# Kernel tuning notes

Hardware: AMD Instinct MI355X
Metric: run time of the kernel (lower is better)

The kernel has to match this reference:

```python
import jax, jax.numpy as jnp
import numpy as np

N_NODES = 50000
N_EDGES = 800000
D = 128


def gcn_conv(x, W, b, src, dst, num_nodes):
    """PyG GCNConv: x @ W, add self-loops, symmetric normalization, scatter-add, + bias."""
    x = x @ W  # [N, out]
    loop = jnp.arange(num_nodes, dtype=src.dtype)
    s = jnp.concatenate([src, loop])  # [E+N]
    d = jnp.concatenate([dst, loop])
    w = jnp.ones(s.shape[0], x.dtype)  # edge_weight=None -> ones (self-loop fill=1)
    deg = jax.ops.segment_sum(w, d, num_segments=num_nodes)  # [N]
    dinv = jnp.where(deg > 0, jax.lax.rsqrt(deg), 0.0)
    norm = dinv[s] * dinv[d]  # [E+N]
    out = jax.ops.segment_sum(x[s] * norm[:, None], d, num_segments=num_nodes)
    return out + b


def setup_inputs() -> dict:
    key = jax.random.key(0)
    ks = jax.random.split(key, 8)
    sc = 1.0 / np.sqrt(D)
    x = jax.random.normal(ks[0], (N_NODES, D), dtype=jnp.float32)
    edge_index = jax.random.randint(ks[1], (2, N_EDGES), 0, N_NODES)
    W1 = jax.random.normal(ks[2], (D, D), dtype=jnp.float32) * sc
    W2 = jax.random.normal(ks[3], (D, D), dtype=jnp.float32) * sc
    W3 = jax.random.normal(ks[4], (D, D), dtype=jnp.float32) * sc
    b1 = jnp.zeros((D,), jnp.float32)
    b2 = jnp.zeros((D,), jnp.float32)
    b3 = jnp.zeros((D,), jnp.float32)
    return {"x": x, "edge_index": edge_index, "W1": W1, "b1": b1,
            "W2": W2, "b2": b2, "W3": W3, "b3": b3}


def reference(x, edge_index, W1, b1, W2, b2, W3, b3):
    src, dst = edge_index[0], edge_index[1]
    n = x.shape[0]
    x = jax.nn.relu(gcn_conv(x, W1, b1, src, dst, n))
    x = jax.nn.relu(gcn_conv(x, W2, b2, src, dst, n))
    return gcn_conv(x, W3, b3, src, dst, n)
```

## Files before the change

### kernel.cpp

```cpp
#include <hip/hip_runtime.h>
#include <hip/hip_fp16.h>
#include <math.h>

#define D 128
#define PADH 136

typedef __attribute__((ext_vector_type(8))) _Float16 half8;
typedef __attribute__((ext_vector_type(4))) float f32x4;


__global__ void prep_kernel(const float* __restrict__ W1, const float* __restrict__ W2,
                            const float* __restrict__ W3, __half* __restrict__ WhT,
                            int* __restrict__ cnt, int N) {
    int i = blockIdx.x * blockDim.x + threadIdx.x;
    if (i < 3 * D * D) {
        int l = i >> 14, j = i & 16383, n = j >> 7, k = j & 127;
        const float* W = (l == 0) ? W1 : (l == 1) ? W2 : W3;
        WhT[(size_t)i] = __float2half(W[(size_t)k * D + n]);
    }
    if (i < N) cnt[i] = 0;
}


__global__ void count_rank_kernel(const int* __restrict__ dst, int* __restrict__ cnt,
                                  int* __restrict__ rank, int E) {
    int e0 = (blockIdx.x * blockDim.x + threadIdx.x) * 8;
    if (e0 + 7 < E) {
        int4 da = *(const int4*)(dst + e0);
        int4 db = *(const int4*)(dst + e0 + 4);
        int4 ra, rb;
        ra.x = atomicAdd(&cnt[da.x], 1);
        ra.y = atomicAdd(&cnt[da.y], 1);
        ra.z = atomicAdd(&cnt[da.z], 1);
        ra.w = atomicAdd(&cnt[da.w], 1);
        rb.x = atomicAdd(&cnt[db.x], 1);
        rb.y = atomicAdd(&cnt[db.y], 1);
        rb.z = atomicAdd(&cnt[db.z], 1);
        rb.w = atomicAdd(&cnt[db.w], 1);
        *(int4*)(rank + e0)     = ra;
        *(int4*)(rank + e0 + 4) = rb;
    } else {
        for (int e = e0; e < E; ++e) rank[e] = atomicAdd(&cnt[dst[e]], 1);
    }
}

__global__ __launch_bounds__(1024) void scan_kernel(const int* __restrict__ cnt,
                                                    int* __restrict__ rowptr,
                                                    float* __restrict__ dinv,
                                                    int N) {
    __shared__ int wsum[16];
    int tid  = threadIdx.x;
    int lane = tid & 63;
    int wid  = tid >> 6;
    int C = ((N + 4095) / 4096) * 4;
    int start = tid * C;
    int end   = start + C; if (end > N) end = N;

    int local = 0;
    int i = start;
    for (; i + 3 < end; i += 4) {
        int4 v = *(const int4*)(cnt + i);
        local += v.x + v.y + v.z + v.w;
    }
    for (; i < end; ++i) local += cnt[i];

    int sc = local;
    #pragma unroll
    for (int off = 1; off < 64; off <<= 1) {
        int t = __shfl_up(sc, off, 64);
        if (lane >= off) sc += t;
    }
    if (lane == 63) wsum[wid] = sc;
    __syncthreads();
    if (tid < 16) {
        int w = wsum[tid];
        #pragma unroll
        for (int off = 1; off < 16; off <<= 1) {
            int t = __shfl_up(w, off, 16);
            if (tid >= off) w += t;
        }
        wsum[tid] = w;
    }
    __syncthreads();
    int run = ((wid > 0) ? wsum[wid - 1] : 0) + (sc - local);

    i = start;
    for (; i + 3 < end; i += 4) {
        int4 v = *(const int4*)(cnt + i);
        int4 rp;
        rp.x = run; rp.y = rp.x + v.x; rp.z = rp.y + v.y; rp.w = rp.z + v.z;
        run = rp.w + v.w;
        *(int4*)(rowptr + i) = rp;
        float4 dv;
        dv.x = rsqrtf((float)v.x + 1.0f);
        dv.y = rsqrtf((float)v.y + 1.0f);
        dv.z = rsqrtf((float)v.z + 1.0f);
        dv.w = rsqrtf((float)v.w + 1.0f);
        *(float4*)(dinv + i) = dv;
    }
    for (; i < end; ++i) {
        int v = cnt[i];
        rowptr[i] = run; run += v;
        dinv[i] = rsqrtf((float)v + 1.0f);
    }
    if (tid == 0) rowptr[N] = wsum[15];
}


__device__ __forceinline__ void gather4(const __half* __restrict__ g,
                                        const int* __restrict__ rowptr,
                                        const int* __restrict__ col,
                                        int row, int lane, float* __restrict__ acc) {
    int grp = lane >> 4;
    int l16 = lane & 15;
    int gb  = grp << 4;
    int s = rowptr[row], e = rowptr[row + 1];

    half8 hs = ((const half8*)(g + (size_t)row * D))[l16];
    float a0 = (float)hs[0], a1 = (float)hs[1], a2 = (float)hs[2], a3 = (float)hs[3];
    float a4 = (float)hs[4], a5 = (float)hs[5], a6 = (float)hs[6], a7 = (float)hs[7];
    float b0 = 0.f, b1 = 0.f, b2 = 0.f, b3 = 0.f, b4 = 0.f, b5 = 0.f, b6 = 0.f, b7 = 0.f;

    for (int base = s; base < e; base += 16) {
        int idx = base + l16;
        int myc = (idx < e) ? col[idx] : 0;
        int nb  = min(16, e - base);
        int j = 0;
        for (; j + 8 <= nb; j += 8) {
            int c0 = __shfl(myc, gb + j + 0), c1 = __shfl(myc, gb + j + 1);
            int c2 = __shfl(myc, gb + j + 2), c3 = __shfl(myc, gb + j + 3);
            int c4 = __shfl(myc, gb + j + 4), c5 = __shfl(myc, gb + j + 5);
            int c6 = __shfl(myc, gb + j + 6), c7 = __shfl(myc, gb + j + 7);
            half8 v0 = ((const half8*)(g + (size_t)c0 * D))[l16];
            half8 v1 = ((const half8*)(g + (size_t)c1 * D))[l16];
            half8 v2 = ((const half8*)(g + (size_t)c2 * D))[l16];
            half8 v3 = ((const half8*)(g + (size_t)c3 * D))[l16];
            half8 v4 = ((const half8*)(g + (size_t)c4 * D))[l16];
            half8 v5 = ((const half8*)(g + (size_t)c5 * D))[l16];
            half8 v6 = ((const half8*)(g + (size_t)c6 * D))[l16];
            half8 v7 = ((const half8*)(g + (size_t)c7 * D))[l16];
            a0 += (float)v0[0]; a1 += (float)v0[1]; a2 += (float)v0[2]; a3 += (float)v0[3];
            a4 += (float)v0[4]; a5 += (float)v0[5]; a6 += (float)v0[6]; a7 += (float)v0[7];
            b0 += (float)v1[0]; b1 += (float)v1[1]; b2 += (float)v1[2]; b3 += (float)v1[3];
            b4 += (float)v1[4]; b5 += (float)v1[5]; b6 += (float)v1[6]; b7 += (float)v1[7];
            a0 += (float)v2[0]; a1 += (float)v2[1]; a2 += (float)v2[2]; a3 += (float)v2[3];
            a4 += (float)v2[4]; a5 += (float)v2[5]; a6 += (float)v2[6]; a7 += (float)v2[7];
            b0 += (float)v3[0]; b1 += (float)v3[1]; b2 += (float)v3[2]; b3 += (float)v3[3];
            b4 += (float)v3[4]; b5 += (float)v3[5]; b6 += (float)v3[6]; b7 += (float)v3[7];
            a0 += (float)v4[0]; a1 += (float)v4[1]; a2 += (float)v4[2]; a3 += (float)v4[3];
            a4 += (float)v4[4]; a5 += (float)v4[5]; a6 += (float)v4[6]; a7 += (float)v4[7];
            b0 += (float)v5[0]; b1 += (float)v5[1]; b2 += (float)v5[2]; b3 += (float)v5[3];
            b4 += (float)v5[4]; b5 += (float)v5[5]; b6 += (float)v5[6]; b7 += (float)v5[7];
            a0 += (float)v6[0]; a1 += (float)v6[1]; a2 += (float)v6[2]; a3 += (float)v6[3];
            a4 += (float)v6[4]; a5 += (float)v6[5]; a6 += (float)v6[6]; a7 += (float)v6[7];
            b0 += (float)v7[0]; b1 += (float)v7[1]; b2 += (float)v7[2]; b3 += (float)v7[3];
            b4 += (float)v7[4]; b5 += (float)v7[5]; b6 += (float)v7[6]; b7 += (float)v7[7];
        }
        for (; j + 4 <= nb; j += 4) {
            int c0 = __shfl(myc, gb + j + 0), c1 = __shfl(myc, gb + j + 1);
            int c2 = __shfl(myc, gb + j + 2), c3 = __shfl(myc, gb + j + 3);
            half8 v0 = ((const half8*)(g + (size_t)c0 * D))[l16];
            half8 v1 = ((const half8*)(g + (size_t)c1 * D))[l16];
            half8 v2 = ((const half8*)(g + (size_t)c2 * D))[l16];
            half8 v3 = ((const half8*)(g + (size_t)c3 * D))[l16];
            a0 += (float)v0[0]; a1 += (float)v0[1]; a2 += (float)v0[2]; a3 += (float)v0[3];
            a4 += (float)v0[4]; a5 += (float)v0[5]; a6 += (float)v0[6]; a7 += (float)v0[7];
            b0 += (float)v1[0]; b1 += (float)v1[1]; b2 += (float)v1[2]; b3 += (float)v1[3];
            b4 += (float)v1[4]; b5 += (float)v1[5]; b6 += (float)v1[6]; b7 += (float)v1[7];
            a0 += (float)v2[0]; a1 += (float)v2[1]; a2 += (float)v2[2]; a3 += (float)v2[3];
            a4 += (float)v2[4]; a5 += (float)v2[5]; a6 += (float)v2[6]; a7 += (float)v2[7];
            b0 += (float)v3[0]; b1 += (float)v3[1]; b2 += (float)v3[2]; b3 += (float)v3[3];
            b4 += (float)v3[4]; b5 += (float)v3[5]; b6 += (float)v3[6]; b7 += (float)v3[7];
        }
        for (; j < nb; ++j) {
            int c = __shfl(myc, gb + j);
            half8 v = ((const half8*)(g + (size_t)c * D))[l16];
            a0 += (float)v[0]; a1 += (float)v[1]; a2 += (float)v[2]; a3 += (float)v[3];
            a4 += (float)v[4]; a5 += (float)v[5]; a6 += (float)v[6]; a7 += (float)v[7];
        }
    }
    acc[0] = a0 + b0; acc[1] = a1 + b1; acc[2] = a2 + b2; acc[3] = a3 + b3;
    acc[4] = a4 + b4; acc[5] = a5 + b5; acc[6] = a6 + b6; acc[7] = a7 + b7;
}


__global__ __launch_bounds__(256) void fill_gemm1_kernel(
    const int* __restrict__ src, const int* __restrict__ dst,
    const int* __restrict__ rank, const int* __restrict__ rowptr,
    int* __restrict__ col, int E, int fill_blocks, int N,
    const float* __restrict__ X, const __half* __restrict__ WhT,
    const float* __restrict__ dinv, __half* __restrict__ Y, int M) {
    int tid = threadIdx.x;
    if ((int)blockIdx.x < fill_blocks) {
        int shard = blockIdx.x & 7;
        int sub   = blockIdx.x >> 3;
        int nsub  = fill_blocks >> 3;
        int chunk = (N + 7) >> 3;
        int lo = shard * chunk;
        unsigned span = (unsigned)(min(lo + chunk, N) - lo);
        const int NO = (E + 7) / 8;
        for (int c = sub * 256 + tid; c < NO; c += nsub * 256) {
            int e0 = c * 8;
            if (e0 + 7 < E) {
                int4 da = *(const int4*)(dst + e0);
                int4 db = *(const int4*)(dst + e0 + 4);
                bool i0 = (unsigned)(da.x - lo) < span, i1 = (unsigned)(da.y - lo) < span;
                bool i2 = (unsigned)(da.z - lo) < span, i3 = (unsigned)(da.w - lo) < span;
                bool i4 = (unsigned)(db.x - lo) < span, i5 = (unsigned)(db.y - lo) < span;
                bool i6 = (unsigned)(db.z - lo) < span, i7 = (unsigned)(db.w - lo) < span;
                if (i0 | i1 | i2 | i3 | i4 | i5 | i6 | i7) {
                    int4 ra = *(const int4*)(rank + e0);
                    int4 rb = *(const int4*)(rank + e0 + 4);
                    int4 sa = *(const int4*)(src + e0);
                    int4 sb = *(const int4*)(src + e0 + 4);
                    if (i0) col[rowptr[da.x] + ra.x] = sa.x;
                    if (i1) col[rowptr[da.y] + ra.y] = sa.y;
                    if (i2) col[rowptr[da.z] + ra.z] = sa.z;
                    if (i3) col[rowptr[da.w] + ra.w] = sa.w;
                    if (i4) col[rowptr[db.x] + rb.x] = sb.x;
                    if (i5) col[rowptr[db.y] + rb.y] = sb.y;
                    if (i6) col[rowptr[db.z] + rb.z] = sb.z;
                    if (i7) col[rowptr[db.w] + rb.w] = sb.w;
                }
            } else {
                for (int e = e0; e < E; ++e) {
                    int d = dst[e];
                    if ((unsigned)(d - lo) < span) col[rowptr[d] + rank[e]] = src[e];
                }
            }
        }
        return;
    }
    int bid  = blockIdx.x - fill_blocks;
    int wave = tid >> 6;
    int lane = tid & 63;
    int quad = lane >> 4;
    int l16  = lane & 15;
    int m0   = bid * 64 + wave * 16;
    if (m0 >= M) return;

    f32x4 acc[8];
    #pragma unroll
    for (int t = 0; t < 8; ++t) acc[t] = (f32x4)0.0f;
    const float* xrow = X + (size_t)(m0 + l16) * D;
    #pragma unroll
    for (int ks = 0; ks < 4; ++ks) {
        int k0 = ks * 32 + quad * 8;
        float4 x0 = *(const float4*)(xrow + k0);
        float4 x1 = *(const float4*)(xrow + k0 + 4);
        half8 a;
        a[0] = (_Float16)x0.x; a[1] = (_Float16)x0.y;
        a[2] = (_Float16)x0.z; a[3] = (_Float16)x0.w;
        a[4] = (_Float16)x1.x; a[5] = (_Float16)x1.y;
        a[6] = (_Float16)x1.z; a[7] = (_Float16)x1.w;
        #pragma unroll
        for (int t = 0; t < 8; ++t) {
            half8 b = *(const half8*)(WhT + (size_t)(t * 16 + l16) * D + k0);
            acc[t] = __builtin_amdgcn_mfma_f32_16x16x32_f16(a, b, acc[t], 0, 0, 0);
        }
    }
    float4 dv = *(const float4*)(dinv + m0 + quad * 4);
    float dvs[4] = {dv.x, dv.y, dv.z, dv.w};
    #pragma unroll
    for (int t = 0; t < 8; ++t) {
        #pragma unroll
        for (int r = 0; r < 4; ++r) {
            int grow = m0 + quad * 4 + r;
            Y[(size_t)grow * D + t * 16 + l16] = __float2half(acc[t][r] * dvs[r]);
        }
    }
}


__global__ __launch_bounds__(256) void agg_gemm_kernel(
    const __half* __restrict__ ysIn, const int* __restrict__ rowptr,
    const int* __restrict__ col, const float* __restrict__ dinv,
    const float* __restrict__ bias, const __half* __restrict__ WhT,
    __half* __restrict__ ysOut, int M) {
    __shared__ __half lds_h[16 * PADH];
    int tid  = threadIdx.x;
    int wave = tid >> 6;
    int lane = tid & 63;
    int grp  = lane >> 4;
    int l16  = lane & 15;
    int rbase = blockIdx.x * 16;
    int lrow  = wave * 4 + grp;
    int row   = min(rbase + lrow, M - 1);

    float acc8[8];
    gather4(ysIn, rowptr, col, row, lane, acc8);

    float dv = dinv[row];
    float4 bb0 = ((const float4*)bias)[l16 * 2];
    float4 bb1 = ((const float4*)bias)[l16 * 2 + 1];
    half8 hv;
    hv[0] = (_Float16)fmaxf(bb0.x + dv * acc8[0], 0.f);
    hv[1] = (_Float16)fmaxf(bb0.y + dv * acc8[1], 0.f);
    hv[2] = (_Float16)fmaxf(bb0.z + dv * acc8[2], 0.f);
    hv[3] = (_Float16)fmaxf(bb0.w + dv * acc8[3], 0.f);
    hv[4] = (_Float16)fmaxf(bb1.x + dv * acc8[4], 0.f);
    hv[5] = (_Float16)fmaxf(bb1.y + dv * acc8[5], 0.f);
    hv[6] = (_Float16)fmaxf(bb1.z + dv * acc8[6], 0.f);
    hv[7] = (_Float16)fmaxf(bb1.w + dv * acc8[7], 0.f);
    ((half8*)(lds_h + (size_t)lrow * PADH))[l16] = hv;
    __syncthreads();

    int quad = lane >> 4;
    int t0   = wave * 2;
    f32x4 acc0 = (f32x4)0.0f, acc1 = (f32x4)0.0f;
    const __half* arow = lds_h + (size_t)l16 * PADH;
    #pragma unroll
    for (int ks = 0; ks < 4; ++ks) {
        int k0 = ks * 32 + quad * 8;
        half8 a  = *(const half8*)(arow + k0);
        half8 b0 = *(const half8*)(WhT + (size_t)((t0 + 0) * 16 + l16) * D + k0);
        half8 b1 = *(const half8*)(WhT + (size_t)((t0 + 1) * 16 + l16) * D + k0);
        acc0 = __builtin_amdgcn_mfma_f32_16x16x32_f16(a, b0, acc0, 0, 0, 0);
        acc1 = __builtin_amdgcn_mfma_f32_16x16x32_f16(a, b1, acc1, 0, 0, 0);
    }
    #pragma unroll
    for (int r = 0; r < 4; ++r) {
        int grow = rbase + quad * 4 + r;
        if (grow < M) {
            float dvr = dinv[grow];
            ysOut[(size_t)grow * D + (t0 + 0) * 16 + l16] = __float2half(acc0[r] * dvr);
            ysOut[(size_t)grow * D + (t0 + 1) * 16 + l16] = __float2half(acc1[r] * dvr);
        }
    }
}


__global__ __launch_bounds__(256) void agg_final_kernel(
    const __half* __restrict__ ys, const int* __restrict__ rowptr,
    const int* __restrict__ col, const float* __restrict__ dinv,
    const float* __restrict__ b, float* __restrict__ out, int N) {
    int gwave = (blockIdx.x * blockDim.x + threadIdx.x) >> 6;
    int lane  = threadIdx.x & 63;
    int grp   = lane >> 4;
    int l16   = lane & 15;
    int rbase = gwave * 4;
    if (rbase >= N) return;
    int row = min(rbase + grp, N - 1);

    float acc8[8];
    gather4(ys, rowptr, col, row, lane, acc8);

    if (rbase + grp < N) {
        float dv = dinv[row];
        float4 bb0 = ((const float4*)b)[l16 * 2];
        float4 bb1 = ((const float4*)b)[l16 * 2 + 1];
        float4 r0, r1;
        r0.x = bb0.x + dv * acc8[0];
        r0.y = bb0.y + dv * acc8[1];
        r0.z = bb0.z + dv * acc8[2];
        r0.w = bb0.w + dv * acc8[3];
        r1.x = bb1.x + dv * acc8[4];
        r1.y = bb1.y + dv * acc8[5];
        r1.z = bb1.z + dv * acc8[6];
        r1.w = bb1.w + dv * acc8[7];
        float* op = out + (size_t)row * D + l16 * 8;
        ((float4*)op)[0] = r0;
        ((float4*)op)[1] = r1;
    }
}


extern "C" void kernel_launch(void* const* d_in, const int* in_sizes, int n_in,
                              void* d_out, int out_size, void* d_ws, size_t ws_size,
                              hipStream_t stream) {
    const float* x   = (const float*)d_in[0];
    const int*   ei  = (const int*)d_in[1];
    const float* W1  = (const float*)d_in[2];
    const float* b1  = (const float*)d_in[3];
    const float* W2  = (const float*)d_in[4];
    const float* b2  = (const float*)d_in[5];
    const float* W3  = (const float*)d_in[6];
    const float* b3  = (const float*)d_in[7];
    float* out = (float*)d_out;

    const int N = in_sizes[0] / D;
    const int E = in_sizes[1] / 2;
    const int* src = ei;
    const int* dst = ei + E;

    char* ws = (char*)d_ws;
    size_t off = 0;
    auto alloc = [&](size_t bytes) {
        void* p = ws + off;
        off = (off + bytes + 255) & ~(size_t)255;
        return p;
    };
    __half* ys    = (__half*)alloc((size_t)N * D * sizeof(__half));
    __half* hs    = (__half*)alloc((size_t)N * D * sizeof(__half));
    int*   cnt    = (int*)alloc((size_t)N * sizeof(int));
    int*   rowptr = (int*)alloc((size_t)(N + 1) * sizeof(int));
    float* dinv   = (float*)alloc((size_t)N * sizeof(float));
    int*   rank   = (int*)alloc((size_t)E * sizeof(int));
    int*   col    = (int*)alloc((size_t)E * sizeof(int));
    __half* WhT   = (__half*)alloc((size_t)3 * D * D * sizeof(__half));
    (void)ws_size; (void)n_in; (void)out_size;

    int prep_threads = (3 * D * D > N) ? 3 * D * D : N;
    prep_kernel<<<(prep_threads + 255) / 256, 256, 0, stream>>>(W1, W2, W3, WhT, cnt, N);

    const int NO = (E + 7) / 8;
    const int egrid = (NO + 255) / 256;
    count_rank_kernel<<<egrid, 256, 0, stream>>>(dst, cnt, rank, E);
    scan_kernel<<<1, 1024, 0, stream>>>(cnt, rowptr, dinv, N);

    const int FB = ((egrid + 7) / 8) * 8;
    const int gemm1_grid = (N + 63) / 64;
    fill_gemm1_kernel<<<FB + gemm1_grid, 256, 0, stream>>>(
        src, dst, rank, rowptr, col, E, FB, N, x, WhT, dinv, ys, N);

    const int agg_gemm_grid = (N + 15) / 16;
    agg_gemm_kernel<<<agg_gemm_grid, 256, 0, stream>>>(ys, rowptr, col, dinv, b1, WhT + 16384, hs, N);
    agg_gemm_kernel<<<agg_gemm_grid, 256, 0, stream>>>(hs, rowptr, col, dinv, b2, WhT + 32768, ys, N);

    const int aggf_grid = (((N + 3) / 4) * 64 + 255) / 256;
    agg_final_kernel<<<aggf_grid, 256, 0, stream>>>(ys, rowptr, col, dinv, b3, out, N);
}
```

Measured before the change: 298.0 us.

## Overlap first-layer GEMM with degree counting and unroll gather by sixteen

Moves the layer-1 X@W1 GEMM into the same launch as the edge degree-count atomics. It writes an fp32 intermediate, and a later fill kernel scales that intermediate by dinv and converts it to fp16 alongside the CSR fill. This lets the GEMM overlap the atomic counting phase instead of waiting for the scan. The gather loop also handles full 16-neighbor batches with 16 outstanding loads. The cost is an extra fp32 N×D buffer round trip, and the new path is used only when the workspace is large enough.

Result: slower. 310.3 us (+4.1%).

```diff
diff --git a/kernel.cpp b/kernel.cpp
--- a/kernel.cpp
+++ b/kernel.cpp
@@ -19,6 +19,405 @@
         WhT[(size_t)i] = __float2half(W[(size_t)k * D + n]);
     }
     if (i < N) cnt[i] = 0;
+}
+
+
+__global__ __launch_bounds__(256) void count_gemm1_kernel(
+    const int* __restrict__ dst, int* __restrict__ cnt, int* __restrict__ rank,
+    int E, int count_blocks,
+    const float* __restrict__ X, const __half* __restrict__ WhT,
+    float* __restrict__ Yf, int M) {
+    int tid = threadIdx.x;
+    if ((int)blockIdx.x < count_blocks) {
+        const int NO = (E + 7) / 8;
+        const int stride = count_blocks * 256;
+        for (int c = blockIdx.x * 256 + tid; c < NO; c += stride) {
+            int e0 = c * 8;
+            if (e0 + 7 < E) {
+                int4 da = *(const int4*)(dst + e0);
+                int4 db = *(const int4*)(dst + e0 + 4);
+                int4 ra, rb;
+                ra.x = atomicAdd(&cnt[da.x], 1);
+                ra.y = atomicAdd(&cnt[da.y], 1);
+                ra.z = atomicAdd(&cnt[da.z], 1);
+                ra.w = atomicAdd(&cnt[da.w], 1);
+                rb.x = atomicAdd(&cnt[db.x], 1);
+                rb.y = atomicAdd(&cnt[db.y], 1);
+                rb.z = atomicAdd(&cnt[db.z], 1);
+                rb.w = atomicAdd(&cnt[db.w], 1);
+                *(int4*)(rank + e0)     = ra;
+                *(int4*)(rank + e0 + 4) = rb;
+            } else {
+                for (int e = e0; e < E; ++e) rank[e] = atomicAdd(&cnt[dst[e]], 1);
+            }
+        }
+        return;
+    }
+    int bid  = blockIdx.x - count_blocks;
+    int wave = tid >> 6;
+    int lane = tid & 63;
+    int quad = lane >> 4;
+    int l16  = lane & 15;
+    int m0   = bid * 64 + wave * 16;
+    if (m0 >= M) return;
+
+    f32x4 acc[8];
+    #pragma unroll
+    for (int t = 0; t < 8; ++t) acc[t] = (f32x4)0.0f;
+    const float* xrow = X + (size_t)(m0 + l16) * D;
+    #pragma unroll
+    for (int ks = 0; ks < 4; ++ks) {
+        int k0 = ks * 32 + quad * 8;
+        float4 x0 = *(const float4*)(xrow + k0);
+        float4 x1 = *(const float4*)(xrow + k0 + 4);
+        half8 a;
+        a[0] = (_Float16)x0.x; a[1] = (_Float16)x0.y;
+        a[2] = (_Float16)x0.z; a[3] = (_Float16)x0.w;
+        a[4] = (_Float16)x1.x; a[5] = (_Float16)x1.y;
+        a[6] = (_Float16)x1.z; a[7] = (_Float16)x1.w;
+        #pragma unroll
+        for (int t = 0; t < 8; ++t) {
+            half8 b = *(const half8*)(WhT + (size_t)(t * 16 + l16) * D + k0);
+            acc[t] = __builtin_amdgcn_mfma_f32_16x16x32_f16(a, b, acc[t], 0, 0, 0);
+        }
+    }
+    #pragma unroll
+    for (int t = 0; t < 8; ++t) {
+        #pragma unroll
+        for (int r = 0; r < 4; ++r) {
+            int grow = m0 + quad * 4 + r;
+            Yf[(size_t)grow * D + t * 16 + l16] = acc[t][r];
+        }
+    }
+}
+
+
+__global__ __launch_bounds__(1024) void scan_kernel(const int* __restrict__ cnt,
+                                                    int* __restrict__ rowptr,
+                                                    float* __restrict__ dinv,
+                                                    int N) {
+    __shared__ int wsum[16];
+    int tid  = threadIdx.x;
+    int lane = tid & 63;
+    int wid  = tid >> 6;
+    int C = ((N + 4095) / 4096) * 4;
+    int start = tid * C;
+    int end   = start + C; if (end > N) end = N;
+
+    int local = 0;
+    int i = start;
+    for (; i + 3 < end; i += 4) {
+        int4 v = *(const int4*)(cnt + i);
+        local += v.x + v.y + v.z + v.w;
+    }
+    for (; i < end; ++i) local += cnt[i];
+
+    int sc = local;
+    #pragma unroll
+    for (int off = 1; off < 64; off <<= 1) {
+        int t = __shfl_up(sc, off, 64);
+        if (lane >= off) sc += t;
+    }
+    if (lane == 63) wsum[wid] = sc;
+    __syncthreads();
+    if (tid < 16) {
+        int w = wsum[tid];
+        #pragma unroll
+        for (int off = 1; off < 16; off <<= 1) {
+            int t = __shfl_up(w, off, 16);
+            if (tid >= off) w += t;
+        }
+        wsum[tid] = w;
+    }
+    __syncthreads();
+    int run = ((wid > 0) ? wsum[wid - 1] : 0) + (sc - local);
+
+    i = start;
+    for (; i + 3 < end; i += 4) {
+        int4 v = *(const int4*)(cnt + i);
+        int4 rp;
+        rp.x = run; rp.y = rp.x + v.x; rp.z = rp.y + v.y; rp.w = rp.z + v.z;
+        run = rp.w + v.w;
+        *(int4*)(rowptr + i) = rp;
+        float4 dv;
+        dv.x = rsqrtf((float)v.x + 1.0f);
+        dv.y = rsqrtf((float)v.y + 1.0f);
+        dv.z = rsqrtf((float)v.z + 1.0f);
+        dv.w = rsqrtf((float)v.w + 1.0f);
+        *(float4*)(dinv + i) = dv;
+    }
+    for (; i < end; ++i) {
+        int v = cnt[i];
+        rowptr[i] = run; run += v;
+        dinv[i] = rsqrtf((float)v + 1.0f);
+    }
+    if (tid == 0) rowptr[N] = wsum[15];
+}
+
+
+__global__ __launch_bounds__(256) void fill_scale_kernel(
+    const int* __restrict__ src, const int* __restrict__ dst,
+    const int* __restrict__ rank, const int* __restrict__ rowptr,
+    int* __restrict__ col, int E, int fill_blocks, int N,
+    const float* __restrict__ Yf, const float* __restrict__ dinv,
+    __half* __restrict__ Y, int scale_blocks) {
+    int tid = threadIdx.x;
+    if ((int)blockIdx.x < fill_blocks) {
+        int shard = blockIdx.x & 7;
+        int sub   = blockIdx.x >> 3;
+        int nsub  = fill_blocks >> 3;
+        int chunk = (N + 7) >> 3;
+        int lo = shard * chunk;
+        unsigned span = (unsigned)(min(lo + chunk, N) - lo);
+        const int NO = (E + 7) / 8;
+        for (int c = sub * 256 + tid; c < NO; c += nsub * 256) {
+            int e0 = c * 8;
+            if (e0 + 7 < E) {
+                int4 da = *(const int4*)(dst + e0);
+                int4 db = *(const int4*)(dst + e0 + 4);
+                bool i0 = (unsigned)(da.x - lo) < span, i1 = (unsigned)(da.y - lo) < span;
+                bool i2 = (unsigned)(da.z - lo) < span, i3 = (unsigned)(da.w - lo) < span;
+                bool i4 = (unsigned)(db.x - lo) < span, i5 = (unsigned)(db.y - lo) < span;
+                bool i6 = (unsigned)(db.z - lo) < span, i7 = (unsigned)(db.w - lo) < span;
+                if (i0 | i1 | i2 | i3 | i4 | i5 | i6 | i7) {
+                    int4 ra = *(const int4*)(rank + e0);
+                    int4 rb = *(const int4*)(rank + e0 + 4);
+                    int4 sa = *(const int4*)(src + e0);
+                    int4 sb = *(const int4*)(src + e0 + 4);
+                    if (i0) col[rowptr[da.x] + ra.x] = sa.x;
+                    if (i1) col[rowptr[da.y] + ra.y] = sa.y;
+                    if (i2) col[rowptr[da.z] + ra.z] = sa.z;
+                    if (i3) col[rowptr[da.w] + ra.w] = sa.w;
+                    if (i4) col[rowptr[db.x] + rb.x] = sb.x;
+                    if (i5) col[rowptr[db.y] + rb.y] = sb.y;
+                    if (i6) col[rowptr[db.z] + rb.z] = sb.z;
+                    if (i7) col[rowptr[db.w] + rb.w] = sb.w;
+                }
+            } else {
+                for (int e = e0; e < E; ++e) {
+                    int d = dst[e];
+                    if ((unsigned)(d - lo) < span) col[rowptr[d] + rank[e]] = src[e];
+                }
+            }
+        }
+        return;
+    }
+    int sb = blockIdx.x - fill_blocks;
+    const int nchunk = N * 16;
+    const int stride = scale_blocks * 256;
+    for (int i = sb * 256 + tid; i < nchunk; i += stride) {
+        int row = i >> 4;
+        int c8  = (i & 15) * 8;
+        const float* p = Yf + (size_t)row * D + c8;
+        float4 x0 = *(const float4*)p;
+        float4 x1 = *(const float4*)(p + 4);
+        float dv = dinv[row];
+        half8 h;
+        h[0] = (_Float16)(x0.x * dv); h[1] = (_Float16)(x0.y * dv);
+        h[2] = (_Float16)(x0.z * dv); h[3] = (_Float16)(x0.w * dv);
+        h[4] = (_Float16)(x1.x * dv); h[5] = (_Float16)(x1.y * dv);
+        h[6] = (_Float16)(x1.z * dv); h[7] = (_Float16)(x1.w * dv);
+        *(half8*)(Y + (size_t)row * D + c8) = h;
+    }
+}
+
+
+__device__ __forceinline__ void gather4(const __half* __restrict__ g,
+                                        const int* __restrict__ rowptr,
+                                        const int* __restrict__ col,
+                                        int row, int lane, float* __restrict__ acc) {
+    int grp = lane >> 4;
+    int l16 = lane & 15;
+    int gb  = grp << 4;
+    int s = rowptr[row], e = rowptr[row + 1];
+
+    half8 hs = ((const half8*)(g + (size_t)row * D))[l16];
+    float a0 = (float)hs[0], a1 = (float)hs[1], a2 = (float)hs[2], a3 = (float)hs[3];
+    float a4 = (float)hs[4], a5 = (float)hs[5], a6 = (float)hs[6], a7 = (float)hs[7];
+    float b0 = 0.f, b1 = 0.f, b2 = 0.f, b3 = 0.f, b4 = 0.f, b5 = 0.f, b6 = 0.f, b7 = 0.f;
+
+    for (int base = s; base < e; base += 16) {
+        int idx = base + l16;
+        int myc = (idx < e) ? col[idx] : 0;
+        int nb  = min(16, e - base);
+        if (nb == 16) {
+            int c0 = __shfl(myc, gb + 0),  c1 = __shfl(myc, gb + 1);
+            int c2 = __shfl(myc, gb + 2),  c3 = __shfl(myc, gb + 3);
+            int c4 = __shfl(myc, gb + 4),  c5 = __shfl(myc, gb + 5);
+            int c6 = __shfl(myc, gb + 6),  c7 = __shfl(myc, gb + 7);
+            int c8 = __shfl(myc, gb + 8),  c9 = __shfl(myc, gb + 9);
+            int cA = __shfl(myc, gb + 10), cB = __shfl(myc, gb + 11);
+            int cC = __shfl(myc, gb + 12), cD = __shfl(myc, gb + 13);
+            int cE = __shfl(myc, gb + 14), cF = __shfl(myc, gb + 15);
+            half8 v0 = ((const half8*)(g + (size_t)c0 * D))[l16];
+            half8 v1 = ((const half8*)(g + (size_t)c1 * D))[l16];
+            half8 v2 = ((const half8*)(g + (size_t)c2 * D))[l16];
+            half8 v3 = ((const half8*)(g + (size_t)c3 * D))[l16];
+            half8 v4 = ((const half8*)(g + (size_t)c4 * D))[l16];
+            half8 v5 = ((const half8*)(g + (size_t)c5 * D))[l16];
+            half8 v6 = ((const half8*)(g + (size_t)c6 * D))[l16];
+            half8 v7 = ((const half8*)(g + (size_t)c7 * D))[l16];
+            half8 v8 = ((const half8*)(g + (size_t)c8 * D))[l16];
+            half8 v9 = ((const half8*)(g + (size_t)c9 * D))[l16];
+            half8 vA = ((const half8*)(g + (size_t)cA * D))[l16];
+            half8 vB = ((const half8*)(g + (size_t)cB * D))[l16];
+            half8 vC = ((const half8*)(g + (size_t)cC * D))[l16];
+            half8 vD = ((const half8*)(g + (size_t)cD * D))[l16];
+            half8 vE = ((const half8*)(g + (size_t)cE * D))[l16];
+            half8 vF = ((const half8*)(g + (size_t)cF * D))[l16];
+            a0 += (float)v0[0]; a1 += (float)v0[1]; a2 += (float)v0[2]; a3 += (float)v0[3];
+            a4 += (float)v0[4]; a5 += (float)v0[5]; a6 += (float)v0[6]; a7 += (float)v0[7];
+            b0 += (float)v1[0]; b1 += (float)v1[1]; b2 += (float)v1[2]; b3 += (float)v1[3];
+            b4 += (float)v1[4]; b5 += (float)v1[5]; b6 += (float)v1[6]; b7 += (float)v1[7];
+            a0 += (float)v2[0]; a1 += (float)v2[1]; a2 += (float)v2[2]; a3 += (float)v2[3];
+            a4 += (float)v2[4]; a5 += (float)v2[5]; a6 += (float)v2[6]; a7 += (float)v2[7];
+            b0 += (float)v3[0]; b1 += (float)v3[1]; b2 += (float)v3[2]; b3 += (float)v3[3];
+            b4 += (float)v3[4]; b5 += (float)v3[5]; b6 += (float)v3[6]; b7 += (float)v3[7];
+            a0 += (float)v4[0]; a1 += (float)v4[1]; a2 += (float)v4[2]; a3 += (float)v4[3];
+            a4 += (float)v4[4]; a5 += (float)v4[5]; a6 += (float)v4[6]; a7 += (float)v4[7];
+            b0 += (float)v5[0]; b1 += (float)v5[1]; b2 += (float)v5[2]; b3 += (float)v5[3];
+            b4 += (float)v5[4]; b5 += (float)v5[5]; b6 += (float)v5[6]; b7 += (float)v5[7];
+            a0 += (float)v6[0]; a1 += (float)v6[1]; a2 += (float)v6[2]; a3 += (float)v6[3];
+            a4 += (float)v6[4]; a5 += (float)v6[5]; a6 += (float)v6[6]; a7 += (float)v6[7];
+            b0 += (float)v7[0]; b1 += (float)v7[1]; b2 += (float)v7[2]; b3 += (float)v7[3];
+            b4 += (float)v7[4]; b5 += (float)v7[5]; b6 += (float)v7[6]; b7 += (float)v7[7];
+            a0 += (float)v8[0]; a1 += (float)v8[1]; a2 += (float)v8[2]; a3 += (float)v8[3];
+            a4 += (float)v8[4]; a5 += (float)v8[5]; a6 += (float)v8[6]; a7 += (float)v8[7];
+            b0 += (float)v9[0]; b1 += (float)v9[1]; b2 += (float)v9[2]; b3 += (float)v9[3];
+            b4 += (float)v9[4]; b5 += (float)v9[5]; b6 += (float)v9[6]; b7 += (float)v9[7];
+            a0 += (float)vA[0]; a1 += (float)vA[1]; a2 += (float)vA[2]; a3 += (float)vA[3];
+            a4 += (float)vA[4]; a5 += (float)vA[5]; a6 += (float)vA[6]; a7 += (float)vA[7];
+            b0 += (float)vB[0]; b1 += (float)vB[1]; b2 += (float)vB[2]; b3 += (float)vB[3];
+            b4 += (float)vB[4]; b5 += (float)vB[5]; b6 += (float)vB[6]; b7 += (float)vB[7];
+            a0 += (float)vC[0]; a1 += (float)vC[1]; a2 += (float)vC[2]; a3 += (float)vC[3];
+            a4 += (float)vC[4]; a5 += (float)vC[5]; a6 += (float)vC[6]; a7 += (float)vC[7];
+            b0 += (float)vD[0]; b1 += (float)vD[1]; b2 += (float)vD[2]; b3 += (float)vD[3];
+            b4 += (float)vD[4]; b5 += (float)vD[5]; b6 += (float)vD[6]; b7 += (float)vD[7];
+            a0 += (float)vE[0]; a1 += (float)vE[1]; a2 += (float)vE[2]; a3 += (float)vE[3];
+            a4 += (float)vE[4]; a5 += (float)vE[5]; a6 += (float)vE[6]; a7 += (float)vE[7];
+            b0 += (float)vF[0]; b1 += (float)vF[1]; b2 += (float)vF[2]; b3 += (float)vF[3];
+            b4 += (float)vF[4]; b5 += (float)vF[5]; b6 += (float)vF[6]; b7 += (float)vF[7];
+        } else {
+            int j = 0;
+            for (; j + 4 <= nb; j += 4) {
+                int c0 = __shfl(myc, gb + j + 0), c1 = __shfl(myc, gb + j + 1);
+                int c2 = __shfl(myc, gb + j + 2), c3 = __shfl(myc, gb + j + 3);
+                half8 v0 = ((const half8*)(g + (size_t)c0 * D))[l16];
+                half8 v1 = ((const half8*)(g + (size_t)c1 * D))[l16];
+                half8 v2 = ((const half8*)(g + (size_t)c2 * D))[l16];
+                half8 v3 = ((const half8*)(g + (size_t)c3 * D))[l16];
+                a0 += (float)v0[0]; a1 += (float)v0[1]; a2 += (float)v0[2]; a3 += (float)v0[3];
+                a4 += (float)v0[4]; a5 += (float)v0[5]; a6 += (float)v0[6]; a7 += (float)v0[7];
+                b0 += (float)v1[0]; b1 += (float)v1[1]; b2 += (float)v1[2]; b3 += (float)v1[3];
+                b4 += (float)v1[4]; b5 += (float)v1[5]; b6 += (float)v1[6]; b7 += (float)v1[7];
+                a0 += (float)v2[0]; a1 += (float)v2[1]; a2 += (float)v2[2]; a3 += (float)v2[3];
+                a4 += (float)v2[4]; a5 += (float)v2[5]; a6 += (float)v2[6]; a7 += (float)v2[7];
+                b0 += (float)v3[0]; b1 += (float)v3[1]; b2 += (float)v3[2]; b3 += (float)v3[3];
+                b4 += (float)v3[4]; b5 += (float)v3[5]; b6 += (float)v3[6]; b7 += (float)v3[7];
+            }
+            for (; j < nb; ++j) {
+                int c = __shfl(myc, gb + j);
+                half8 v = ((const half8*)(g + (size_t)c * D))[l16];
+                a0 += (float)v[0]; a1 += (float)v[1]; a2 += (float)v[2]; a3 += (float)v[3];
+                a4 += (float)v[4]; a5 += (float)v[5]; a6 += (float)v[6]; a7 += (float)v[7];
+            }
+        }
+    }
+    acc[0] = a0 + b0; acc[1] = a1 + b1; acc[2] = a2 + b2; acc[3] = a3 + b3;
+    acc[4] = a4 + b4; acc[5] = a5 + b5; acc[6] = a6 + b6; acc[7] = a7 + b7;
+}
+
+
+__global__ __launch_bounds__(256) void agg_gemm_kernel(
+    const __half* __restrict__ ysIn, const int* __restrict__ rowptr,
+    const int* __restrict__ col, const float* __restrict__ dinv,
+    const float* __restrict__ bias, const __half* __restrict__ WhT,
+    __half* __restrict__ ysOut, int M) {
+    __shared__ __half lds_h[16 * PADH];
+    int tid  = threadIdx.x;
+    int wave = tid >> 6;
+    int lane = tid & 63;
+    int grp  = lane >> 4;
+    int l16  = lane & 15;
+    int rbase = blockIdx.x * 16;
+    int lrow  = wave * 4 + grp;
+    int row   = min(rbase + lrow, M - 1);
+
+    float acc8[8];
+    gather4(ysIn, rowptr, col, row, lane, acc8);
+
+    float dv = dinv[row];
+    float4 bb0 = ((const float4*)bias)[l16 * 2];
+    float4 bb1 = ((const float4*)bias)[l16 * 2 + 1];
+    half8 hv;
+    hv[0] = (_Float16)fmaxf(bb0.x + dv * acc8[0], 0.f);
+    hv[1] = (_Float16)fmaxf(bb0.y + dv * acc8[1], 0.f);
+    hv[2] = (_Float16)fmaxf(bb0.z + dv * acc8[2], 0.f);
+    hv[3] = (_Float16)fmaxf(bb0.w + dv * acc8[3], 0.f);
+    hv[4] = (_Float16)fmaxf(bb1.x + dv * acc8[4], 0.f);
+    hv[5] = (_Float16)fmaxf(bb1.y + dv * acc8[5], 0.f);
+    hv[6] = (_Float16)fmaxf(bb1.z + dv * acc8[6], 0.f);
+    hv[7] = (_Float16)fmaxf(bb1.w + dv * acc8[7], 0.f);
+    ((half8*)(lds_h + (size_t)lrow * PADH))[l16] = hv;
+    __syncthreads();
+
+    int quad = lane >> 4;
+    int t0   = wave * 2;
+    f32x4 acc0 = (f32x4)0.0f, acc1 = (f32x4)0.0f;
+    const __half* arow = lds_h + (size_t)l16 * PADH;
+    #pragma unroll
+    for (int ks = 0; ks < 4; ++ks) {
+        int k0 = ks * 32 + quad * 8;
+        half8 a  = *(const half8*)(arow + k0);
+        half8 b0 = *(const half8*)(WhT + (size_t)((t0 + 0) * 16 + l16) * D + k0);
+        half8 b1 = *(const half8*)(WhT + (size_t)((t0 + 1) * 16 + l16) * D + k0);
+        acc0 = __builtin_amdgcn_mfma_f32_16x16x32_f16(a, b0, acc0, 0, 0, 0);
+        acc1 = __builtin_amdgcn_mfma_f32_16x16x32_f16(a, b1, acc1, 0, 0, 0);
+    }
+    #pragma unroll
+    for (int r = 0; r < 4; ++r) {
+        int grow = rbase + quad * 4 + r;
+        if (grow < M) {
+            float dvr = dinv[grow];
+            ysOut[(size_t)grow * D + (t0 + 0) * 16 + l16] = __float2half(acc0[r] * dvr);
+            ysOut[(size_t)grow * D + (t0 + 1) * 16 + l16] = __float2half(acc1[r] * dvr);
+        }
+    }
+}
+
+
+__global__ __launch_bounds__(256) void agg_final_kernel(
+    const __half* __restrict__ ys, const int* __restrict__ rowptr,
+    const int* __restrict__ col, const float* __restrict__ dinv,
+    const float* __restrict__ b, float* __restrict__ out, int N) {
+    int gwave = (blockIdx.x * blockDim.x + threadIdx.x) >> 6;
+    int lane  = threadIdx.x & 63;
+    int grp   = lane >> 4;
+    int l16   = lane & 15;
+    int rbase = gwave * 4;
+    if (rbase >= N) return;
+    int row = min(rbase + grp, N - 1);
+
+    float acc8[8];
+    gather4(ys, rowptr, col, row, lane, acc8);
+
+    if (rbase + grp < N) {
+        float dv = dinv[row];
+        float4 bb0 = ((const float4*)b)[l16 * 2];
+        float4 bb1 = ((const float4*)b)[l16 * 2 + 1];
+        float4 r0, r1;
+        r0.x = bb0.x + dv * acc8[0];
+        r0.y = bb0.y + dv * acc8[1];
+        r0.z = bb0.z + dv * acc8[2];
+        r0.w = bb0.w + dv * acc8[3];
+        r1.x = bb1.x + dv * acc8[4];
+        r1.y = bb1.y + dv * acc8[5];
+        r1.z = bb1.z + dv * acc8[6];
+        r1.w = bb1.w + dv * acc8[7];
+        float* op = out + (size_t)row * D + l16 * 8;
+        ((float4*)op)[0] = r0;
+        ((float4*)op)[1] = r1;
+    }
 }
 
 
@@ -43,146 +442,6 @@
         for (int e = e0; e < E; ++e) rank[e] = atomicAdd(&cnt[dst[e]], 1);
     }
 }
-
-__global__ __launch_bounds__(1024) void scan_kernel(const int* __restrict__ cnt,
-                                                    int* __restrict__ rowptr,
-                                                    float* __restrict__ dinv,
-                                                    int N) {
-    __shared__ int wsum[16];
-    int tid  = threadIdx.x;
-    int lane = tid & 63;
-    int wid  = tid >> 6;
-    int C = ((N + 4095) / 4096) * 4;
-    int start = tid * C;
-    int end   = start + C; if (end > N) end = N;
-
-    int local = 0;
-    int i = start;
-    for (; i + 3 < end; i += 4) {
-        int4 v = *(const int4*)(cnt + i);
-        local += v.x + v.y + v.z + v.w;
-    }
-    for (; i < end; ++i) local += cnt[i];
-
-    int sc = local;
-    #pragma unroll
-    for (int off = 1; off < 64; off <<= 1) {
-        int t = __shfl_up(sc, off, 64);
-        if (lane >= off) sc += t;
-    }
-    if (lane == 63) wsum[wid] = sc;
-    __syncthreads();
-    if (tid < 16) {
-        int w = wsum[tid];
-        #pragma unroll
-        for (int off = 1; off < 16; off <<= 1) {
-            int t = __shfl_up(w, off, 16);
-            if (tid >= off) w += t;
-        }
-        wsum[tid] = w;
-    }
-    __syncthreads();
-    int run = ((wid > 0) ? wsum[wid - 1] : 0) + (sc - local);
-
-    i = start;
-    for (; i + 3 < end; i += 4) {
-        int4 v = *(const int4*)(cnt + i);
-        int4 rp;
-        rp.x = run; rp.y = rp.x + v.x; rp.z = rp.y + v.y; rp.w = rp.z + v.z;
-        run = rp.w + v.w;
-        *(int4*)(rowptr + i) = rp;
-        float4 dv;
-        dv.x = rsqrtf((float)v.x + 1.0f);
-        dv.y = rsqrtf((float)v.y + 1.0f);
-        dv.z = rsqrtf((float)v.z + 1.0f);
-        dv.w = rsqrtf((float)v.w + 1.0f);
-        *(float4*)(dinv + i) = dv;
-    }
-    for (; i < end; ++i) {
-        int v = cnt[i];
-        rowptr[i] = run; run += v;
-        dinv[i] = rsqrtf((float)v + 1.0f);
-    }
-    if (tid == 0) rowptr[N] = wsum[15];
-}
-
-
-__device__ __forceinline__ void gather4(const __half* __restrict__ g,
-                                        const int* __restrict__ rowptr,
-                                        const int* __restrict__ col,
-                                        int row, int lane, float* __restrict__ acc) {
-    int grp = lane >> 4;
-    int l16 = lane & 15;
-    int gb  = grp << 4;
-    int s = rowptr[row], e = rowptr[row + 1];
-
-    half8 hs = ((const half8*)(g + (size_t)row * D))[l16];
-    float a0 = (float)hs[0], a1 = (float)hs[1], a2 = (float)hs[2], a3 = (float)hs[3];
-    float a4 = (float)hs[4], a5 = (float)hs[5], a6 = (float)hs[6], a7 = (float)hs[7];
-    float b0 = 0.f, b1 = 0.f, b2 = 0.f, b3 = 0.f, b4 = 0.f, b5 = 0.f, b6 = 0.f, b7 = 0.f;
-
-    for (int base = s; base < e; base += 16) {
-        int idx = base + l16;
-        int myc = (idx < e) ? col[idx] : 0;
-        int nb  = min(16, e - base);
-        int j = 0;
-        for (; j + 8 <= nb; j += 8) {
-            int c0 = __shfl(myc, gb + j + 0), c1 = __shfl(myc, gb + j + 1);
-            int c2 = __shfl(myc, gb + j + 2), c3 = __shfl(myc, gb + j + 3);
-            int c4 = __shfl(myc, gb + j + 4), c5 = __shfl(myc, gb + j + 5);
-            int c6 = __shfl(myc, gb + j + 6), c7 = __shfl(myc, gb + j + 7);
-            half8 v0 = ((const half8*)(g + (size_t)c0 * D))[l16];
-            half8 v1 = ((const half8*)(g + (size_t)c1 * D))[l16];
-            half8 v2 = ((const half8*)(g + (size_t)c2 * D))[l16];
-            half8 v3 = ((const half8*)(g + (size_t)c3 * D))[l16];
-            half8 v4 = ((const half8*)(g + (size_t)c4 * D))[l16];
-            half8 v5 = ((const half8*)(g + (size_t)c5 * D))[l16];
-            half8 v6 = ((const half8*)(g + (size_t)c6 * D))[l16];
-            half8 v7 = ((const half8*)(g + (size_t)c7 * D))[l16];
-            a0 += (float)v0[0]; a1 += (float)v0[1]; a2 += (float)v0[2]; a3 += (float)v0[3];
-            a4 += (float)v0[4]; a5 += (float)v0[5]; a6 += (float)v0[6]; a7 += (float)v0[7];
-            b0 += (float)v1[0]; b1 += (float)v1[1]; b2 += (float)v1[2]; b3 += (float)v1[3];
-            b4 += (float)v1[4]; b5 += (float)v1[5]; b6 += (float)v1[6]; b7 += (float)v1[7];
-            a0 += (float)v2[0]; a1 += (float)v2[1]; a2 += (float)v2[2]; a3 += (float)v2[3];
-            a4 += (float)v2[4]; a5 += (float)v2[5]; a6 += (float)v2[6]; a7 += (float)v2[7];
-            b0 += (float)v3[0]; b1 += (float)v3[1]; b2 += (float)v3[2]; b3 += (float)v3[3];
-            b4 += (float)v3[4]; b5 += (float)v3[5]; b6 += (float)v3[6]; b7 += (float)v3[7];
-            a0 += (float)v4[0]; a1 += (float)v4[1]; a2 += (float)v4[2]; a3 += (float)v4[3];
-            a4 += (float)v4[4]; a5 += (float)v4[5]; a6 += (float)v4[6]; a7 += (float)v4[7];
-            b0 += (float)v5[0]; b1 += (float)v5[1]; b2 += (float)v5[2]; b3 += (float)v5[3];
-            b4 += (float)v5[4]; b5 += (float)v5[5]; b6 += (float)v5[6]; b7 += (float)v5[7];
-            a0 += (float)v6[0]; a1 += (float)v6[1]; a2 += (float)v6[2]; a3 += (float)v6[3];
-            a4 += (float)v6[4]; a5 += (float)v6[5]; a6 += (float)v6[6]; a7 += (float)v6[7];
-            b0 += (float)v7[0]; b1 += (float)v7[1]; b2 += (float)v7[2]; b3 += (float)v7[3];
-            b4 += (float)v7[4]; b5 += (float)v7[5]; b6 += (float)v7[6]; b7 += (float)v7[7];
-        }
-        for (; j + 4 <= nb; j += 4) {
-            int c0 = __shfl(myc, gb + j + 0), c1 = __shfl(myc, gb + j + 1);
-            int c2 = __shfl(myc, gb + j + 2), c3 = __shfl(myc, gb + j + 3);
-            half8 v0 = ((const half8*)(g + (size_t)c0 * D))[l16];
-            half8 v1 = ((const half8*)(g + (size_t)c1 * D))[l16];
-            half8 v2 = ((const half8*)(g + (size_t)c2 * D))[l16];
-            half8 v3 = ((const half8*)(g + (size_t)c3 * D))[l16];
-            a0 += (float)v0[0]; a1 += (float)v0[1]; a2 += (float)v0[2]; a3 += (float)v0[3];
-            a4 += (float)v0[4]; a5 += (float)v0[5]; a6 += (float)v0[6]; a7 += (float)v0[7];
-            b0 += (float)v1[0]; b1 += (float)v1[1]; b2 += (float)v1[2]; b3 += (float)v1[3];
-            b4 += (float)v1[4]; b5 += (float)v1[5]; b6 += (float)v1[6]; b7 += (float)v1[7];
-            a0 += (float)v2[0]; a1 += (float)v2[1]; a2 += (float)v2[2]; a3 += (float)v2[3];
-            a4 += (float)v2[4]; a5 += (float)v2[5]; a6 += (float)v2[6]; a7 += (float)v2[7];
-            b0 += (float)v3[0]; b1 += (float)v3[1]; b2 += (float)v3[2]; b3 += (float)v3[3];
-            b4 += (float)v3[4]; b5 += (float)v3[5]; b6 += (float)v3[6]; b7 += (float)v3[7];
-        }
-        for (; j < nb; ++j) {
-            int c = __shfl(myc, gb + j);
-            half8 v = ((const half8*)(g + (size_t)c * D))[l16];
-            a0 += (float)v[0]; a1 += (float)v[1]; a2 += (float)v[2]; a3 += (float)v[3];
-            a4 += (float)v[4]; a5 += (float)v[5]; a6 += (float)v[6]; a7 += (float)v[7];
-        }
-    }
-    acc[0] = a0 + b0; acc[1] = a1 + b1; acc[2] = a2 + b2; acc[3] = a3 + b3;
-    acc[4] = a4 + b4; acc[5] = a5 + b5; acc[6] = a6 + b6; acc[7] = a7 + b7;
-}
-
 
 __global__ __launch_bounds__(256) void fill_gemm1_kernel(
     const int* __restrict__ src, const int* __restrict__ dst,
@@ -272,99 +531,6 @@
 }
 
 
-__global__ __launch_bounds__(256) void agg_gemm_kernel(
-    const __half* __restrict__ ysIn, const int* __restrict__ rowptr,
-    const int* __restrict__ col, const float* __restrict__ dinv,
-    const float* __restrict__ bias, const __half* __restrict__ WhT,
-    __half* __restrict__ ysOut, int M) {
-    __shared__ __half lds_h[16 * PADH];
-    int tid  = threadIdx.x;
-    int wave = tid >> 6;
-    int lane = tid & 63;
-    int grp  = lane >> 4;
-    int l16  = lane & 15;
-    int rbase = blockIdx.x * 16;
-    int lrow  = wave * 4 + grp;
-    int row   = min(rbase + lrow, M - 1);
-
-    float acc8[8];
-    gather4(ysIn, rowptr, col, row, lane, acc8);
-
-    float dv = dinv[row];
-    float4 bb0 = ((const float4*)bias)[l16 * 2];
-    float4 bb1 = ((const float4*)bias)[l16 * 2 + 1];
-    half8 hv;
-    hv[0] = (_Float16)fmaxf(bb0.x + dv * acc8[0], 0.f);
-    hv[1] = (_Float16)fmaxf(bb0.y + dv * acc8[1], 0.f);
-    hv[2] = (_Float16)fmaxf(bb0.z + dv * acc8[2], 0.f);
-    hv[3] = (_Float16)fmaxf(bb0.w + dv * acc8[3], 0.f);
-    hv[4] = (_Float16)fmaxf(bb1.x + dv * acc8[4], 0.f);
-    hv[5] = (_Float16)fmaxf(bb1.y + dv * acc8[5], 0.f);
-    hv[6] = (_Float16)fmaxf(bb1.z + dv * acc8[6], 0.f);
-    hv[7] = (_Float16)fmaxf(bb1.w + dv * acc8[7], 0.f);
-    ((half8*)(lds_h + (size_t)lrow * PADH))[l16] = hv;
-    __syncthreads();
-
-    int quad = lane >> 4;
-    int t0   = wave * 2;
-    f32x4 acc0 = (f32x4)0.0f, acc1 = (f32x4)0.0f;
-    const __half* arow = lds_h + (size_t)l16 * PADH;
-    #pragma unroll
-    for (int ks = 0; ks < 4; ++ks) {
-        int k0 = ks * 32 + quad * 8;
-        half8 a  = *(const half8*)(arow + k0);
-        half8 b0 = *(const half8*)(WhT + (size_t)((t0 + 0) * 16 + l16) * D + k0);
-        half8 b1 = *(const half8*)(WhT + (size_t)((t0 + 1) * 16 + l16) * D + k0);
-        acc0 = __builtin_amdgcn_mfma_f32_16x16x32_f16(a, b0, acc0, 0, 0, 0);
-        acc1 = __builtin_amdgcn_mfma_f32_16x16x32_f16(a, b1, acc1, 0, 0, 0);
-    }
-    #pragma unroll
-    for (int r = 0; r < 4; ++r) {
-        int grow = rbase + quad * 4 + r;
-        if (grow < M) {
-            float dvr = dinv[grow];
-            ysOut[(size_t)grow * D + (t0 + 0) * 16 + l16] = __float2half(acc0[r] * dvr);
-            ysOut[(size_t)grow * D + (t0 + 1) * 16 + l16] = __float2half(acc1[r] * dvr);
-        }
-    }
-}
-
-
-__global__ __launch_bounds__(256) void agg_final_kernel(
-    const __half* __restrict__ ys, const int* __restrict__ rowptr,
-    const int* __restrict__ col, const float* __restrict__ dinv,
-    const float* __restrict__ b, float* __restrict__ out, int N) {
-    int gwave = (blockIdx.x * blockDim.x + threadIdx.x) >> 6;
-    int lane  = threadIdx.x & 63;
-    int grp   = lane >> 4;
-    int l16   = lane & 15;
-    int rbase = gwave * 4;
-    if (rbase >= N) return;
-    int row = min(rbase + grp, N - 1);
-
-    float acc8[8];
-    gather4(ys, rowptr, col, row, lane, acc8);
-
-    if (rbase + grp < N) {
-        float dv = dinv[row];
-        float4 bb0 = ((const float4*)b)[l16 * 2];
-        float4 bb1 = ((const float4*)b)[l16 * 2 + 1];
-        float4 r0, r1;
-        r0.x = bb0.x + dv * acc8[0];
-        r0.y = bb0.y + dv * acc8[1];
-        r0.z = bb0.z + dv * acc8[2];
-        r0.w = bb0.w + dv * acc8[3];
-        r1.x = bb1.x + dv * acc8[4];
-        r1.y = bb1.y + dv * acc8[5];
-        r1.z = bb1.z + dv * acc8[6];
-        r1.w = bb1.w + dv * acc8[7];
-        float* op = out + (size_t)row * D + l16 * 8;
-        ((float4*)op)[0] = r0;
-        ((float4*)op)[1] = r1;
-    }
-}
-
-
 extern "C" void kernel_launch(void* const* d_in, const int* in_sizes, int n_in,
                               void* d_out, int out_size, void* d_ws, size_t ws_size,
                               hipStream_t stream) {
@@ -398,20 +564,34 @@
     int*   rank   = (int*)alloc((size_t)E * sizeof(int));
     int*   col    = (int*)alloc((size_t)E * sizeof(int));
     __half* WhT   = (__half*)alloc((size_t)3 * D * D * sizeof(__half));
-    (void)ws_size; (void)n_in; (void)out_size;
+    size_t base_need = off;
+    float* ysf    = (float*)alloc((size_t)N * D * sizeof(float));
+    size_t full_need = off;
+    (void)n_in; (void)out_size; (void)base_need;
+
+    const bool planA = (ws_size == 0) || (ws_size >= full_need);
 
     int prep_threads = (3 * D * D > N) ? 3 * D * D : N;
     prep_kernel<<<(prep_threads + 255) / 256, 256, 0, stream>>>(W1, W2, W3, WhT, cnt, N);
 
     const int NO = (E + 7) / 8;
     const int egrid = (NO + 255) / 256;
-    count_rank_kernel<<<egrid, 256, 0, stream>>>(dst, cnt, rank, E);
-    scan_kernel<<<1, 1024, 0, stream>>>(cnt, rowptr, dinv, N);
-
+    const int gemm1_grid = (N + 63) / 64;
     const int FB = ((egrid + 7) / 8) * 8;
-    const int gemm1_grid = (N + 63) / 64;
-    fill_gemm1_kernel<<<FB + gemm1_grid, 256, 0, stream>>>(
-        src, dst, rank, rowptr, col, E, FB, N, x, WhT, dinv, ys, N);
+
+    if (planA) {
+        count_gemm1_kernel<<<egrid + gemm1_grid, 256, 0, stream>>>(
+            dst, cnt, rank, E, egrid, x, WhT, ysf, N);
+        scan_kernel<<<1, 1024, 0, stream>>>(cnt, rowptr, dinv, N);
+        const int SB = 256;
+        fill_scale_kernel<<<FB + SB, 256, 0, stream>>>(
+            src, dst, rank, rowptr, col, E, FB, N, ysf, dinv, ys, SB);
+    } else {
+        count_rank_kernel<<<egrid, 256, 0, stream>>>(dst, cnt, rank, E);
+        scan_kernel<<<1, 1024, 0, stream>>>(cnt, rowptr, dinv, N);
+        fill_gemm1_kernel<<<FB + gemm1_grid, 256, 0, stream>>>(
+            src, dst, rank, rowptr, col, E, FB, N, x, WhT, dinv, ys, N);
+    }
 
     const int agg_gemm_grid = (N + 15) / 16;
     agg_gemm_kernel<<<agg_gemm_grid, 256, 0, stream>>>(ys, rowptr, col, dinv, b1, WhT + 16384, hs, N);
```
